# Kernel optimization log

Measured on AMD Instinct MI355X. Metric: run time of the kernel, lower is better.

## Reference

```python
import jax, jax.numpy as jnp
import numpy as np

B, N, F, H, OUT = 64, 512, 128, 256, 6


def setup_inputs() -> dict:
    key = jax.random.key(0)
    ks = jax.random.split(key, 20)
    s = 0.02
    inp = {
        "x": jax.random.normal(ks[0], (B * N, F), dtype=jnp.float32),
        "edge_index": jax.random.randint(ks[1], (2, 16), 0, B * N),
        "edge_weight": jax.random.uniform(ks[2], (16,), dtype=jnp.float32),
        "batch": jnp.repeat(jnp.arange(B, dtype=jnp.int64), N),
        "sigma": jax.random.uniform(ks[3], (1,), dtype=jnp.float32),
        "Wg": s * jax.random.normal(ks[4], (F, F)), "bg": jnp.zeros((F,)),
        "Wrel0": s * jax.random.normal(ks[5], (F, H)), "Wroot0": s * jax.random.normal(ks[6], (F, H)), "brel0": jnp.zeros((H,)),
        "Wrel1": s * jax.random.normal(ks[7], (H, H)), "Wroot1": s * jax.random.normal(ks[8], (H, H)), "brel1": jnp.zeros((H,)),
        "Wrel2": s * jax.random.normal(ks[9], (H, H)), "Wroot2": s * jax.random.normal(ks[10], (H, H)), "brel2": jnp.zeros((H,)),
        "W1": s * jax.random.normal(ks[11], (H, H)), "b1": jnp.zeros((H,)),
        "Wout": s * jax.random.normal(ks[12], (H, OUT)), "bout": jnp.zeros((OUT,)),
    }
    return inp


def _forward(x, sigma, Wg, bg, Wrel0, Wroot0, brel0, Wrel1, Wroot1, brel1,
             Wrel2, Wroot2, brel2, W1, b1, Wout, bout):
    # gdmLinear
    h = x @ Wg + bg                      # [B*N, F]
    hw = h.reshape(B, N, -1)             # to_dense_batch (equal-size windows)
    # pairwise squared distances per window -> Gaussian kernel
    sq = jnp.sum(hw * hw, axis=-1)       # [B, N]
    dist = jnp.maximum(sq[:, :, None] + sq[:, None, :]
                       - 2.0 * jnp.einsum('bnf,bmf->bnm', hw, hw), 0.0)
    A = jnp.exp(-dist / (2.0 * sigma[0] ** 2))   # [B, N, N], all > 0
    A = A * (1.0 - jnp.eye(N, dtype=A.dtype))    # nonzero extraction drops self-loops

    def conv(h, Wrel, Wroot, brel):
        # GraphConv: out_i = W_rel @ sum_j A[j,i] * h_j + b_rel + W_root @ h_i
        agg = jnp.einsum('bji,bjf->bif', A, h)
        return agg @ Wrel + brel + h @ Wroot

    h = hw
    h = jax.nn.relu(conv(h, Wrel0, Wroot0, brel0))
    h = jax.nn.relu(conv(h, Wrel1, Wroot1, brel1))
    h = conv(h, Wrel2, Wroot2, brel2)
    g = jnp.mean(h, axis=1)              # global_mean_pool (equal-size graphs)
    g = jax.nn.relu(g @ W1 + b1)
    return g @ Wout + bout               # [B, OUT]


def reference(x, edge_index, edge_weight, batch, sigma, Wg, bg,
              Wrel0, Wroot0, brel0, Wrel1, Wroot1, brel1,
              Wrel2, Wroot2, brel2, W1, b1, Wout, bout):
    # edge_index / edge_weight / batch inputs are recomputed internally by GdmGNN
    return _forward(x, sigma, Wg, bg, Wrel0, Wroot0, brel0, Wrel1, Wroot1, brel1,
                    Wrel2, Wroot2, brel2, W1, b1, Wout, bout)
```

## Files before the change

### kernel.cpp

```cpp
#include <hip/hip_runtime.h>
#include <math.h>

#define Bsz 64
#define Nn 512
#define Ff 128
#define Hh 256
#define OUTD 6
#define MTOT (Bsz * Nn)

typedef __bf16 bf16x8 __attribute__((ext_vector_type(8)));
typedef float f32x4 __attribute__((ext_vector_type(4)));
typedef int int4v __attribute__((ext_vector_type(4)));
typedef unsigned short ushort4v __attribute__((ext_vector_type(4)));

__device__ __forceinline__ unsigned short f2bf(float f) {
    unsigned u = __float_as_uint(f);
    u += 0x7FFFu + ((u >> 16) & 1u);
    return (unsigned short)(u >> 16);
}
__device__ __forceinline__ float bf2f(unsigned short s) {
    return __uint_as_float(((unsigned)s) << 16);
}

#define SWZ(r) (((r) ^ ((r) >> 2)) & 3)

__device__ __forceinline__ void async_ld16(const unsigned short* g, unsigned short* l) {
    __builtin_amdgcn_global_load_lds(
        (const __attribute__((address_space(1))) void*)g,
        (__attribute__((address_space(3))) void*)l,
        16, 0, 0);
}

#define LDH 40
#define TSZ (128 * 32)
#define ATS (256 * 32)
#define AGP 136
#define AGP1 264

__global__ __launch_bounds__(512) void fused_l0(
    const unsigned short* __restrict__ h0T,
    const unsigned short* __restrict__ Arows,
    const unsigned short* __restrict__ h0b,
    const unsigned short* __restrict__ WrelT0,
    const unsigned short* __restrict__ WrootT0,
    const float* __restrict__ brel0,
    unsigned short* __restrict__ h1b,
    unsigned short* __restrict__ h1T)
{
    int id = blockIdx.x;
    int b = id & 63;
    int nt = id >> 6;
    int n0g = nt * 128;
    long nodeBase = (long)b * Nn + n0g;

    const unsigned short* HT = h0T + (long)b * Ff * Nn;
    const unsigned short* AR = Arows + (long)b * Nn * Nn;

    __shared__ unsigned short SA[2 * ATS];
    __shared__ unsigned short SB[2 * TSZ];
    __shared__ unsigned short aggL[128 * AGP];

    int tid = threadIdx.x;
    int lane = tid & 63;
    int wave = tid >> 6;
    int quad = lane >> 4, l16 = lane & 15;
    int sr = lane >> 2, sc = lane & 3;

    {
        int wm = (wave >> 1) * 32, wn = (wave & 1) * 64;
        f32x4 acc[2][4] = {};
        auto issue = [&](int g) {
            int kk = g << 5;
            unsigned short* Ad = SA + (g & 1) * ATS;
            unsigned short* Bd = SB + (g & 1) * TSZ;
            int r = wave * 16 + sr;
            int c = sc ^ SWZ(r);
            async_ld16(HT + (long)r * Nn + kk + c * 8, Ad + (wave * 16) * 32);
            async_ld16(AR + (long)(n0g + r) * Nn + kk + c * 8, Bd + (wave * 16) * 32);
        };
        issue(0);
        for (int g = 0; g < (Nn >> 5); ++g) {
            __syncthreads();
            if (g + 1 < (Nn >> 5)) issue(g + 1);
            const unsigned short* Ab = SA + (g & 1) * ATS;
            const unsigned short* Bb = SB + (g & 1) * TSZ;
            bf16x8 af[2], bfr[4];
            #pragma unroll
            for (int i = 0; i < 2; ++i) {
                int r = wm + i * 16 + l16;
                af[i] = *(const bf16x8*)&Ab[r * 32 + (quad ^ SWZ(r)) * 8];
            }
            #pragma unroll
            for (int j = 0; j < 4; ++j) {
                int r = wn + j * 16 + l16;
                bfr[j] = *(const bf16x8*)&Bb[r * 32 + (quad ^ SWZ(r)) * 8];
            }
            #pragma unroll
            for (int i = 0; i < 2; ++i)
                #pragma unroll
                for (int j = 0; j < 4; ++j)
                    acc[i][j] = __builtin_amdgcn_mfma_f32_16x16x32_bf16(
                        af[i], bfr[j], acc[i][j], 0, 0, 0);
        }
        #pragma unroll
        for (int i = 0; i < 2; ++i) {
            int f = wm + i * 16 + quad * 4;
            #pragma unroll
            for (int j = 0; j < 4; ++j) {
                int nl = wn + j * 16 + l16;
                f32x4 v = acc[i][j];
                ushort4v p;
                p[0] = f2bf(v[0]); p[1] = f2bf(v[1]);
                p[2] = f2bf(v[2]); p[3] = f2bf(v[3]);
                *(ushort4v*)&aggL[nl * AGP + f] = p;
            }
        }
    }
    __syncthreads();

    {
        int wm = (wave >> 1) * 64, wn = (wave & 1) * 64;
        f32x4 acc[4][4] = {};
        auto issue2 = [&](int g) {
            const unsigned short* Wp = (g < 4) ? WrelT0 : WrootT0;
            int kk = (g & 3) << 5;
            unsigned short* Ad = SA + (g & 1) * ATS;
            int r = wave * 16 + sr;
            int c = sc ^ SWZ(r);
            async_ld16(Wp + (long)r * Ff + kk + c * 8, Ad + (wave * 16) * 32);
            int r2 = 128 + r;
            int c2 = sc ^ SWZ(r2);
            async_ld16(Wp + (long)r2 * Ff + kk + c2 * 8, Ad + (128 + wave * 16) * 32);
            if (g >= 4) {
                unsigned short* Bd = SB + (g & 1) * TSZ;
                async_ld16(h0b + (nodeBase + r) * Ff + kk + c * 8,
                           Bd + (wave * 16) * 32);
            }
        };
        issue2(0);
        for (int g = 0; g < 8; ++g) {
            __syncthreads();
            if (g + 1 < 8) issue2(g + 1);
            const unsigned short* Ab = SA + (g & 1) * ATS;
            bf16x8 af[4], bfr[4];
            #pragma unroll
            for (int i = 0; i < 4; ++i) {
                int r = wm + i * 16 + l16;
                af[i] = *(const bf16x8*)&Ab[r * 32 + (quad ^ SWZ(r)) * 8];
            }
            if (g < 4) {
                #pragma unroll
                for (int j = 0; j < 4; ++j) {
                    int nl = wn + j * 16 + l16;
                    bfr[j] = *(const bf16x8*)&aggL[nl * AGP + (g << 5) + quad * 8];
                }
            } else {
                const unsigned short* Bb = SB + (g & 1) * TSZ;
                #pragma unroll
                for (int j = 0; j < 4; ++j) {
                    int r = wn + j * 16 + l16;
                    bfr[j] = *(const bf16x8*)&Bb[r * 32 + (quad ^ SWZ(r)) * 8];
                }
            }
            #pragma unroll
            for (int i = 0; i < 4; ++i)
                #pragma unroll
                for (int j = 0; j < 4; ++j)
                    acc[i][j] = __builtin_amdgcn_mfma_f32_16x16x32_bf16(
                        af[i], bfr[j], acc[i][j], 0, 0, 0);
        }
        #pragma unroll
        for (int i = 0; i < 4; ++i) {
            int of = wm + i * 16 + quad * 4;
            float b0 = brel0[of + 0], b1 = brel0[of + 1];
            float b2 = brel0[of + 2], b3 = brel0[of + 3];
            #pragma unroll
            for (int j = 0; j < 4; ++j) {
                int nl = wn + j * 16 + l16;
                f32x4 v = acc[i][j];
                float o0 = fmaxf(v[0] + b0, 0.f), o1 = fmaxf(v[1] + b1, 0.f);
                float o2 = fmaxf(v[2] + b2, 0.f), o3 = fmaxf(v[3] + b3, 0.f);
                ushort4v p;
                p[0] = f2bf(o0); p[1] = f2bf(o1); p[2] = f2bf(o2); p[3] = f2bf(o3);
                *(ushort4v*)&h1b[(nodeBase + nl) * Hh + of] = p;
                long base = ((long)b * Hh) * 512 + n0g + nl;
                h1T[base + (long)(of + 0) * 512] = p[0];
                h1T[base + (long)(of + 1) * 512] = p[1];
                h1T[base + (long)(of + 2) * 512] = p[2];
                h1T[base + (long)(of + 3) * 512] = p[3];
            }
        }
    }
}

__global__ __launch_bounds__(512) void fused_l1(
    const unsigned short* __restrict__ h1T,
    const unsigned short* __restrict__ Arows,
    const unsigned short* __restrict__ h1b,
    const unsigned short* __restrict__ WrelT1,
    const unsigned short* __restrict__ WrootT1,
    const float* __restrict__ brel1,
    const float* __restrict__ w,
    float* __restrict__ vpart, float* __restrict__ mpart)
{
    constexpr int BTS = 128 * 32;

    int id = blockIdx.x;
    int b = id & 63;
    int nt = id >> 6;
    int n0g = nt * 128;
    long nodeBase = (long)b * Nn + n0g;

    const unsigned short* HT = h1T + (long)b * Hh * Nn;
    const unsigned short* AR = Arows + (long)b * Nn * Nn;

    __shared__ unsigned short SA[2 * ATS];
    __shared__ unsigned short SB[2 * BTS];
    __shared__ unsigned short aggL[128 * AGP1];

    int tid = threadIdx.x;
    int lane = tid & 63;
    int wave = tid >> 6;
    int quad = lane >> 4, l16 = lane & 15;
    int wm = (wave >> 1) * 64;
    int wn = (wave & 1) * 64;
    int sr = lane >> 2, sc = lane & 3;

    {
        f32x4 acc[4][4] = {};
        auto issue = [&](int g) {
            int kk = g << 5;
            unsigned short* Ad = SA + (g & 1) * ATS;
            int r = wave * 16 + sr;
            int c = sc ^ SWZ(r);
            async_ld16(HT + (long)r * Nn + kk + c * 8, Ad + (wave * 16) * 32);
            int r2 = 128 + r;
            int c2 = sc ^ SWZ(r2);
            async_ld16(HT + (long)r2 * Nn + kk + c2 * 8, Ad + (128 + wave * 16) * 32);
            unsigned short* Bd = SB + (g & 1) * BTS;
            async_ld16(AR + (long)(n0g + r) * Nn + kk + c * 8, Bd + (wave * 16) * 32);
        };
        issue(0);
        for (int g = 0; g < 16; ++g) {
            __syncthreads();
            if (g + 1 < 16) issue(g + 1);
            const unsigned short* Ab = SA + (g & 1) * ATS;
            const unsigned short* Bb = SB + (g & 1) * BTS;
            bf16x8 af[4], bfr[4];
            #pragma unroll
            for (int i = 0; i < 4; ++i) {
                int r = wm + i * 16 + l16;
                af[i] = *(const bf16x8*)&Ab[r * 32 + (quad ^ SWZ(r)) * 8];
            }
            #pragma unroll
            for (int j = 0; j < 4; ++j) {
                int r = wn + j * 16 + l16;
                bfr[j] = *(const bf16x8*)&Bb[r * 32 + (quad ^ SWZ(r)) * 8];
            }
            #pragma unroll
            for (int i = 0; i < 4; ++i)
                #pragma unroll
                for (int j = 0; j < 4; ++j)
                    acc[i][j] = __builtin_amdgcn_mfma_f32_16x16x32_bf16(
                        af[i], bfr[j], acc[i][j], 0, 0, 0);
        }
        #pragma unroll
        for (int i = 0; i < 4; ++i) {
            int f = wm + i * 16 + quad * 4;
            #pragma unroll
            for (int j = 0; j < 4; ++j) {
                int nl = wn + j * 16 + l16;
                f32x4 v = acc[i][j];
                ushort4v p;
                p[0] = f2bf(v[0]); p[1] = f2bf(v[1]);
                p[2] = f2bf(v[2]); p[3] = f2bf(v[3]);
                *(ushort4v*)&aggL[nl * AGP1 + f] = p;
            }
        }
    }
    __syncthreads();

    f32x4 acc[4][4] = {};
    auto issue2 = [&](int g) {
        const unsigned short* Wp = (g < 8) ? WrelT1 : WrootT1;
        int kk = (g & 7) << 5;
        unsigned short* Ad = SA + (g & 1) * ATS;
        int r = wave * 16 + sr;
        int c = sc ^ SWZ(r);
        async_ld16(Wp + (long)r * Hh + kk + c * 8, Ad + (wave * 16) * 32);
        int r2 = 128 + r;
        int c2 = sc ^ SWZ(r2);
        async_ld16(Wp + (long)r2 * Hh + kk + c2 * 8, Ad + (128 + wave * 16) * 32);
        if (g >= 8) {
            unsigned short* Bd = SB + (g & 1) * BTS;
            async_ld16(h1b + (nodeBase + r) * Hh + kk + c * 8, Bd + (wave * 16) * 32);
        }
    };
    issue2(0);
    for (int g = 0; g < 16; ++g) {
        __syncthreads();
        if (g + 1 < 16) issue2(g + 1);
        const unsigned short* Ab = SA + (g & 1) * ATS;
        bf16x8 af[4], bfr[4];
        #pragma unroll
        for (int i = 0; i < 4; ++i) {
            int r = wm + i * 16 + l16;
            af[i] = *(const bf16x8*)&Ab[r * 32 + (quad ^ SWZ(r)) * 8];
        }
        if (g < 8) {
            #pragma unroll
            for (int j = 0; j < 4; ++j) {
                int nl = wn + j * 16 + l16;
                bfr[j] = *(const bf16x8*)&aggL[nl * AGP1 + (g << 5) + quad * 8];
            }
        } else {
            const unsigned short* Bb = SB + (g & 1) * BTS;
            #pragma unroll
            for (int j = 0; j < 4; ++j) {
                int r = wn + j * 16 + l16;
                bfr[j] = *(const bf16x8*)&Bb[r * 32 + (quad ^ SWZ(r)) * 8];
            }
        }
        #pragma unroll
        for (int i = 0; i < 4; ++i)
            #pragma unroll
            for (int j = 0; j < 4; ++j)
                acc[i][j] = __builtin_amdgcn_mfma_f32_16x16x32_bf16(
                    af[i], bfr[j], acc[i][j], 0, 0, 0);
    }

    #pragma unroll
    for (int i = 0; i < 4; ++i) {
        int lf = wm + i * 16 + quad * 4;
        float b0 = brel1[lf + 0], b1 = brel1[lf + 1];
        float b2 = brel1[lf + 2], b3 = brel1[lf + 3];
        float vp0 = 0.f, vp1 = 0.f, vp2 = 0.f, vp3 = 0.f;
        float mp0 = 0.f, mp1 = 0.f, mp2 = 0.f, mp3 = 0.f;
        #pragma unroll
        for (int j = 0; j < 4; ++j) {
            long node = nodeBase + wn + j * 16 + l16;
            f32x4 v = acc[i][j];
            float o0 = fmaxf(v[0] + b0, 0.f), o1 = fmaxf(v[1] + b1, 0.f);
            float o2 = fmaxf(v[2] + b2, 0.f), o3 = fmaxf(v[3] + b3, 0.f);
            float h0v = bf2f(f2bf(o0)), h1v = bf2f(f2bf(o1));
            float h2v = bf2f(f2bf(o2)), h3v = bf2f(f2bf(o3));
            float wv = w[node];
            vp0 += wv * h0v; vp1 += wv * h1v; vp2 += wv * h2v; vp3 += wv * h3v;
            mp0 += h0v; mp1 += h1v; mp2 += h2v; mp3 += h3v;
        }
        #pragma unroll
        for (int m = 1; m < 16; m <<= 1) {
            vp0 += __shfl_xor(vp0, m); vp1 += __shfl_xor(vp1, m);
            vp2 += __shfl_xor(vp2, m); vp3 += __shfl_xor(vp3, m);
            mp0 += __shfl_xor(mp0, m); mp1 += __shfl_xor(mp1, m);
            mp2 += __shfl_xor(mp2, m); mp3 += __shfl_xor(mp3, m);
        }
        if (l16 == 0) {
            long o = ((long)(b * 8 + nt * 2 + (wave & 1))) * Hh + lf;
            float4 vv = {vp0, vp1, vp2, vp3};
            float4 mm = {mp0, mp1, mp2, mp3};
            *(float4*)&vpart[o] = vv;
            *(float4*)&mpart[o] = mm;
        }
    }
}

__global__ __launch_bounds__(256) void prep_h0(
    const float* __restrict__ x, const float* __restrict__ Wg,
    const float* __restrict__ bg,
    const float* __restrict__ Wrel0, const float* __restrict__ Wroot0,
    const float* __restrict__ Wrel1, const float* __restrict__ Wroot1,
    unsigned short* __restrict__ T0, unsigned short* __restrict__ T1,
    unsigned short* __restrict__ T2, unsigned short* __restrict__ T3,
    float* __restrict__ w,
    unsigned short* __restrict__ h0b, unsigned short* __restrict__ h0T,
    float* __restrict__ sqv)
{
    if (blockIdx.x < 896) {
        int idx = blockIdx.x * 256 + threadIdx.x;
        if (idx >= 196608) { w[idx - 196608] = 0.f; return; }
        const float* src; unsigned short* dst; int kin; int e;
        if      (idx <  32768) { src = Wrel0;  dst = T0; kin = 128; e = idx; }
        else if (idx <  65536) { src = Wroot0; dst = T1; kin = 128; e = idx - 32768; }
        else if (idx < 131072) { src = Wrel1;  dst = T2; kin = 256; e = idx - 65536; }
        else                   { src = Wroot1; dst = T3; kin = 256; e = idx - 131072; }
        int o = (kin == 128) ? (e >> 7) : (e >> 8);
        int i = e & (kin - 1);
        dst[e] = f2bf(src[(long)i * 256 + o]);
        return;
    }

    __shared__ unsigned short As[128 * LDH];
    __shared__ unsigned short Bs[128 * LDH];
    __shared__ float rsq[128];

    int tid = threadIdx.x;
    int lane = tid & 63;
    int wave = tid >> 6;
    int quad = lane >> 4, l16 = lane & 15;
    int wm = (wave >> 1) * 64, wn = (wave & 1) * 64;
    int m0 = (blockIdx.x - 896) * 128;

    f32x4 acc[4][4] = {};

    for (int k0 = 0; k0 < Ff; k0 += 32) {
        __syncthreads();
        #pragma unroll
        for (int l = 0; l < 2; ++l) {
            int idx = tid + l * 256;
            int r = idx >> 2, ch = idx & 3;
            const float* px = x + (long)(m0 + r) * Ff + k0 + ch * 8;
            float4 xa = *(const float4*)px;
            float4 xb = *(const float4*)(px + 4);
            ushort4v pa, pb;
            pa[0] = f2bf(xa.x); pa[1] = f2bf(xa.y); pa[2] = f2bf(xa.z); pa[3] = f2bf(xa.w);
            pb[0] = f2bf(xb.x); pb[1] = f2bf(xb.y); pb[2] = f2bf(xb.z); pb[3] = f2bf(xb.w);
            *(ushort4v*)&As[r * LDH + ch * 8] = pa;
            *(ushort4v*)&As[r * LDH + ch * 8 + 4] = pb;
            int kk = k0 + ch * 8;
            ushort4v qa, qb;
            #pragma unroll
            for (int u = 0; u < 4; ++u) qa[u] = f2bf(Wg[(long)(kk + u) * 128 + r]);
            #pragma unroll
            for (int u = 0; u < 4; ++u) qb[u] = f2bf(Wg[(long)(kk + 4 + u) * 128 + r]);
            *(ushort4v*)&Bs[r * LDH + ch * 8] = qa;
            *(ushort4v*)&Bs[r * LDH + ch * 8 + 4] = qb;
        }
        __syncthreads();
        bf16x8 af[4], bfr[4];
        #pragma unroll
        for (int i = 0; i < 4; ++i)
            af[i] = *(const bf16x8*)&As[(wm + i * 16 + l16) * LDH + quad * 8];
        #pragma unroll
        for (int j = 0; j < 4; ++j)
            bfr[j] = *(const bf16x8*)&Bs[(wn + j * 16 + l16) * LDH + quad * 8];
        #pragma unroll
        for (int i = 0; i < 4; ++i)
            #pragma unroll
            for (int j = 0; j < 4; ++j)
                acc[i][j] = __builtin_amdgcn_mfma_f32_16x16x32_bf16(
                    af[i], bfr[j], acc[i][j], 0, 0, 0);
    }

    if (tid < 128) rsq[tid] = 0.f;
    __syncthreads();

    #pragma unroll
    for (int i = 0; i < 4; ++i) {
        int lrow = wm + i * 16 + quad * 4;
        int mb = m0 + lrow;
        float rp0 = 0.f, rp1 = 0.f, rp2 = 0.f, rp3 = 0.f;
        #pragma unroll
        for (int j = 0; j < 4; ++j) {
            int n = wn + j * 16 + l16;
            f32x4 v = acc[i][j];
            float bv = bg[n];
            unsigned short s0 = f2bf(v[0] + bv), s1 = f2bf(v[1] + bv);
            unsigned short s2 = f2bf(v[2] + bv), s3 = f2bf(v[3] + bv);
            h0b[(long)(mb + 0) * Ff + n] = s0;
            h0b[(long)(mb + 1) * Ff + n] = s1;
            h0b[(long)(mb + 2) * Ff + n] = s2;
            h0b[(long)(mb + 3) * Ff + n] = s3;
            ushort4v p; p[0] = s0; p[1] = s1; p[2] = s2; p[3] = s3;
            long ti = ((long)(mb >> 9) * Ff + n) * 512 + (mb & 511);
            *(ushort4v*)&h0T[ti] = p;
            float f0 = bf2f(s0), f1 = bf2f(s1), f2 = bf2f(s2), f3 = bf2f(s3);
            rp0 += f0 * f0; rp1 += f1 * f1; rp2 += f2 * f2; rp3 += f3 * f3;
        }
        #pragma unroll
        for (int m = 1; m < 16; m <<= 1) {
            rp0 += __shfl_xor(rp0, m);
            rp1 += __shfl_xor(rp1, m);
            rp2 += __shfl_xor(rp2, m);
            rp3 += __shfl_xor(rp3, m);
        }
        if (l16 == 0) {
            atomicAdd(&rsq[lrow + 0], rp0);
            atomicAdd(&rsq[lrow + 1], rp1);
            atomicAdd(&rsq[lrow + 2], rp2);
            atomicAdd(&rsq[lrow + 3], rp3);
        }
    }
    __syncthreads();
    if (tid < 128) sqv[m0 + tid] = rsq[tid];
}

__global__ __launch_bounds__(512) void gram_A_mfma(
    const unsigned short* __restrict__ h0b, const float* __restrict__ sqv,
    const float* __restrict__ sigma, unsigned short* __restrict__ Aout,
    float* __restrict__ w)
{
    int id = blockIdx.x;
    int b = id & 63;
    int t = id >> 6;
    int i0 = (t & 3) * 128, j0 = (t >> 2) * 128;

    const unsigned short* H = h0b + (long)b * Nn * Ff;
    const float* SQ = sqv + (long)b * Nn;
    unsigned short* Ab = Aout + (long)b * Nn * Nn;

    __shared__ unsigned short Is[2 * TSZ];
    __shared__ unsigned short Js[2 * TSZ];
    __shared__ float rsum[128];

    int tid = threadIdx.x;
    int lane = tid & 63;
    int wave = tid >> 6;
    int quad = lane >> 4, l16 = lane & 15;
    int wm = (wave >> 1) * 32, wn = (wave & 1) * 64;

    int sr = lane >> 2, sc = lane & 3;

    f32x4 acc[2][4] = {};

    auto issue = [&](int g) {
        int kk = g << 5;
        unsigned short* Id = Is + (g & 1) * TSZ;
        unsigned short* Jd = Js + (g & 1) * TSZ;
        int r = wave * 16 + sr;
        int c = sc ^ SWZ(r);
        async_ld16(H + (long)(i0 + r) * Ff + kk + c * 8, Id + (wave * 16) * 32);
        async_ld16(H + (long)(j0 + r) * Ff + kk + c * 8, Jd + (wave * 16) * 32);
    };

    issue(0);
    for (int g = 0; g < (Ff >> 5); ++g) {
        __syncthreads();
        if (g + 1 < (Ff >> 5)) issue(g + 1);
        const unsigned short* Ib = Is + (g & 1) * TSZ;
        const unsigned short* Jb = Js + (g & 1) * TSZ;
        bf16x8 af[2], bfr[4];
        #pragma unroll
        for (int i = 0; i < 2; ++i) {
            int r = wm + i * 16 + l16;
            af[i] = *(const bf16x8*)&Ib[r * 32 + (quad ^ SWZ(r)) * 8];
        }
        #pragma unroll
        for (int j = 0; j < 4; ++j) {
            int r = wn + j * 16 + l16;
            bfr[j] = *(const bf16x8*)&Jb[r * 32 + (quad ^ SWZ(r)) * 8];
        }
        #pragma unroll
        for (int i = 0; i < 2; ++i)
            #pragma unroll
            for (int j = 0; j < 4; ++j)
                acc[i][j] = __builtin_amdgcn_mfma_f32_16x16x32_bf16(
                    af[i], bfr[j], acc[i][j], 0, 0, 0);
    }

    if (tid < 128) rsum[tid] = 0.f;
    __syncthreads();

    float s = sigma[0];
    float inv2s2 = 1.0f / (2.0f * s * s);
    #pragma unroll
    for (int i = 0; i < 2; ++i) {
        int lrow = wm + i * 16 + quad * 4;
        int rb = i0 + lrow;
        float rs0 = 0.f, rs1 = 0.f, rs2 = 0.f, rs3 = 0.f;
        #pragma unroll
        for (int j = 0; j < 4; ++j) {
            int c = j0 + wn + j * 16 + l16;
            float sqc = SQ[c];
            f32x4 v = acc[i][j];
            ushort4v pk;
            float av[4];
            #pragma unroll
            for (int r4 = 0; r4 < 4; ++r4) {
                int r = rb + r4;
                float d = fmaxf(SQ[r] + sqc - 2.0f * v[r4], 0.0f);
                unsigned short a = (r == c) ? (unsigned short)0
                                            : f2bf(__expf(-d * inv2s2));
                pk[r4] = a;
                av[r4] = bf2f(a);
            }
            *(ushort4v*)&Ab[(long)c * Nn + rb] = pk;
            rs0 += av[0]; rs1 += av[1]; rs2 += av[2]; rs3 += av[3];
        }
        #pragma unroll
        for (int m = 1; m < 16; m <<= 1) {
            rs0 += __shfl_xor(rs0, m);
            rs1 += __shfl_xor(rs1, m);
            rs2 += __shfl_xor(rs2, m);
            rs3 += __shfl_xor(rs3, m);
        }
        if (l16 == 0) {
            atomicAdd(&rsum[lrow + 0], rs0);
            atomicAdd(&rsum[lrow + 1], rs1);
            atomicAdd(&rsum[lrow + 2], rs2);
            atomicAdd(&rsum[lrow + 3], rs3);
        }
    }
    __syncthreads();
    if (tid < 128) atomicAdd(&w[(long)b * Nn + i0 + tid], rsum[tid]);
}

__global__ __launch_bounds__(256) void head_kernel(
    const float* __restrict__ vpart, const float* __restrict__ mpart,
    const float* __restrict__ Wrel2, const float* __restrict__ Wroot2,
    const float* __restrict__ brel2,
    const float* __restrict__ W1, const float* __restrict__ b1,
    const float* __restrict__ Wout, const float* __restrict__ bout,
    float* __restrict__ out)
{
    int b = blockIdx.x;
    int j = threadIdx.x;
    __shared__ float vs[Hh], ms[Hh], gs[Hh], g2[Hh];
    float vp = 0.f, mp = 0.f;
    #pragma unroll
    for (int p = 0; p < 8; ++p) {
        long o = ((long)(b * 8 + p)) * Hh + j;
        vp += vpart[o];
        mp += mpart[o];
    }
    vs[j] = vp * (1.0f / (float)Nn);
    ms[j] = mp * (1.0f / (float)Nn);
    __syncthreads();
    float s = brel2[j];
    for (int c = 0; c < Hh; ++c)
        s += vs[c] * Wrel2[c * Hh + j] + ms[c] * Wroot2[c * Hh + j];
    gs[j] = s;
    __syncthreads();
    float t = b1[j];
    for (int k = 0; k < Hh; ++k) t += gs[k] * W1[k * Hh + j];
    g2[j] = fmaxf(t, 0.f);
    __syncthreads();
    if (j < OUTD) {
        float s2 = bout[j];
        for (int k = 0; k < Hh; ++k) s2 += g2[k] * Wout[k * OUTD + j];
        out[b * OUTD + j] = s2;
    }
}

extern "C" void kernel_launch(void* const* d_in, const int* in_sizes, int n_in,
                              void* d_out, int out_size, void* d_ws, size_t ws_size,
                              hipStream_t stream) {
    const float* x      = (const float*)d_in[0];
    const float* sigma  = (const float*)d_in[4];
    const float* Wg     = (const float*)d_in[5];
    const float* bg     = (const float*)d_in[6];
    const float* Wrel0  = (const float*)d_in[7];
    const float* Wroot0 = (const float*)d_in[8];
    const float* brel0  = (const float*)d_in[9];
    const float* Wrel1  = (const float*)d_in[10];
    const float* Wroot1 = (const float*)d_in[11];
    const float* brel1  = (const float*)d_in[12];
    const float* Wrel2  = (const float*)d_in[13];
    const float* Wroot2 = (const float*)d_in[14];
    const float* brel2  = (const float*)d_in[15];
    const float* W1     = (const float*)d_in[16];
    const float* b1     = (const float*)d_in[17];
    const float* Wout   = (const float*)d_in[18];
    const float* bout   = (const float*)d_in[19];
    float* out = (float*)d_out;

    char* ws = (char*)d_ws;
    unsigned short* h0b  = (unsigned short*)(ws + 16777216);
    unsigned short* h0T  = (unsigned short*)(ws + 25165824);
    float*          sq   = (float*)(ws + 33554432);
    unsigned short* Aadj = (unsigned short*)(ws + 33685504);
    unsigned short* h1b  = (unsigned short*)(ws + 84017152);
    unsigned short* h1T  = (unsigned short*)(ws + 100794368);
    unsigned short* WrelT0  = (unsigned short*)(ws + 167903232);
    unsigned short* WrootT0 = (unsigned short*)(ws + 167968768);
    unsigned short* WrelT1  = (unsigned short*)(ws + 168034304);
    unsigned short* WrootT1 = (unsigned short*)(ws + 168165376);
    float*          w     = (float*)(ws + 168558592);
    float*          vpart = (float*)(ws + 168689664);
    float*          mpart = (float*)(ws + 169213952);

    prep_h0<<<1152, 256, 0, stream>>>(x, Wg, bg, Wrel0, Wroot0, Wrel1, Wroot1,
                                      WrelT0, WrootT0, WrelT1, WrootT1,
                                      w, h0b, h0T, sq);

    gram_A_mfma<<<dim3(16 * Bsz, 1, 1), 512, 0, stream>>>(h0b, sq, sigma, Aadj, w);

    fused_l0<<<dim3(4 * Bsz, 1, 1), 512, 0, stream>>>(
        h0T, Aadj, h0b, WrelT0, WrootT0, brel0, h1b, h1T);

    fused_l1<<<dim3(4 * Bsz, 1, 1), 512, 0, stream>>>(
        h1T, Aadj, h1b, WrelT1, WrootT1, brel1, w, vpart, mpart);

    head_kernel<<<Bsz, 256, 0, stream>>>(vpart, mpart, Wrel2, Wroot2, brel2,
                                         W1, b1, Wout, bout, out);
}
```

Before: 211.5 us.

## Triple-buffer LDS tiles with explicit vmcnt waits for two-deep prefetch

Turns the double-buffered async global-to-LDS pipelines in the fused GraphConv kernels into triple-buffered ones. Two tiles are now in flight ahead of compute, and the full __syncthreads is replaced by a partial s_waitcnt vmcnt(n) followed by s_barrier. The aim is to hide more global-load latency behind the MFMA work. In exchange, LDS use per block grows, which can lower occupancy, and the hand-counted vmcnt values must match the number of loads issued per stage exactly or data races appear.

```diff
diff --git a/kernel.cpp b/kernel.cpp
--- a/kernel.cpp
+++ b/kernel.cpp
@@ -29,6 +29,23 @@
         (const __attribute__((address_space(1))) void*)g,
         (__attribute__((address_space(3))) void*)l,
         16, 0, 0);
+}
+
+__device__ __forceinline__ void wait_vm(int n) {
+    switch (n) {
+        case 0: asm volatile("s_waitcnt vmcnt(0)" ::: "memory"); break;
+        case 1: asm volatile("s_waitcnt vmcnt(1)" ::: "memory"); break;
+        case 2: asm volatile("s_waitcnt vmcnt(2)" ::: "memory"); break;
+        case 3: asm volatile("s_waitcnt vmcnt(3)" ::: "memory"); break;
+        case 4: asm volatile("s_waitcnt vmcnt(4)" ::: "memory"); break;
+        case 5: asm volatile("s_waitcnt vmcnt(5)" ::: "memory"); break;
+        default: asm volatile("s_waitcnt vmcnt(6)" ::: "memory"); break;
+    }
+}
+__device__ __forceinline__ void pipe_barrier(int n) {
+    wait_vm(n);
+    __builtin_amdgcn_s_barrier();
+    __builtin_amdgcn_sched_barrier(0);
 }
 
 #define LDH 40
@@ -56,8 +73,8 @@
     const unsigned short* HT = h0T + (long)b * Ff * Nn;
     const unsigned short* AR = Arows + (long)b * Nn * Nn;
 
-    __shared__ unsigned short SA[2 * ATS];
-    __shared__ unsigned short SB[2 * TSZ];
+    __shared__ unsigned short SA[3 * ATS];
+    __shared__ unsigned short SB[3 * TSZ];
     __shared__ unsigned short aggL[128 * AGP];
 
     int tid = threadIdx.x;
@@ -71,19 +88,19 @@
         f32x4 acc[2][4] = {};
         auto issue = [&](int g) {
             int kk = g << 5;
-            unsigned short* Ad = SA + (g & 1) * ATS;
-            unsigned short* Bd = SB + (g & 1) * TSZ;
+            unsigned short* Ad = SA + (g % 3) * ATS;
+            unsigned short* Bd = SB + (g % 3) * TSZ;
             int r = wave * 16 + sr;
             int c = sc ^ SWZ(r);
             async_ld16(HT + (long)r * Nn + kk + c * 8, Ad + (wave * 16) * 32);
             async_ld16(AR + (long)(n0g + r) * Nn + kk + c * 8, Bd + (wave * 16) * 32);
         };
-        issue(0);
-        for (int g = 0; g < (Nn >> 5); ++g) {
-            __syncthreads();
-            if (g + 1 < (Nn >> 5)) issue(g + 1);
-            const unsigned short* Ab = SA + (g & 1) * ATS;
-            const unsigned short* Bb = SB + (g & 1) * TSZ;
+        issue(0); issue(1);
+        for (int g = 0; g < 16; ++g) {
+            pipe_barrier(g + 1 < 16 ? 2 : 0);
+            if (g + 2 < 16) issue(g + 2);
+            const unsigned short* Ab = SA + (g % 3) * ATS;
+            const unsigned short* Bb = SB + (g % 3) * TSZ;
             bf16x8 af[2], bfr[4];
             #pragma unroll
             for (int i = 0; i < 2; ++i) {
@@ -124,7 +141,7 @@
         auto issue2 = [&](int g) {
             const unsigned short* Wp = (g < 4) ? WrelT0 : WrootT0;
             int kk = (g & 3) << 5;
-            unsigned short* Ad = SA + (g & 1) * ATS;
+            unsigned short* Ad = SA + (g % 3) * ATS;
             int r = wave * 16 + sr;
             int c = sc ^ SWZ(r);
             async_ld16(Wp + (long)r * Ff + kk + c * 8, Ad + (wave * 16) * 32);
@@ -132,16 +149,17 @@
             int c2 = sc ^ SWZ(r2);
             async_ld16(Wp + (long)r2 * Ff + kk + c2 * 8, Ad + (128 + wave * 16) * 32);
             if (g >= 4) {
-                unsigned short* Bd = SB + (g & 1) * TSZ;
+                unsigned short* Bd = SB + (g % 3) * TSZ;
                 async_ld16(h0b + (nodeBase + r) * Ff + kk + c * 8,
                            Bd + (wave * 16) * 32);
             }
         };
-        issue2(0);
+        issue2(0); issue2(1);
         for (int g = 0; g < 8; ++g) {
-            __syncthreads();
-            if (g + 1 < 8) issue2(g + 1);
-            const unsigned short* Ab = SA + (g & 1) * ATS;
+            int nx = g + 1;
+            pipe_barrier(nx >= 8 ? 0 : (nx < 4 ? 2 : 3));
+            if (g + 2 < 8) issue2(g + 2);
+            const unsigned short* Ab = SA + (g % 3) * ATS;
             bf16x8 af[4], bfr[4];
             #pragma unroll
             for (int i = 0; i < 4; ++i) {
@@ -155,7 +173,7 @@
                     bfr[j] = *(const bf16x8*)&aggL[nl * AGP + (g << 5) + quad * 8];
                 }
             } else {
-                const unsigned short* Bb = SB + (g & 1) * TSZ;
+                const unsigned short* Bb = SB + (g % 3) * TSZ;
                 #pragma unroll
                 for (int j = 0; j < 4; ++j) {
                     int r = wn + j * 16 + l16;
@@ -214,8 +232,8 @@
     const unsigned short* HT = h1T + (long)b * Hh * Nn;
     const unsigned short* AR = Arows + (long)b * Nn * Nn;
 
-    __shared__ unsigned short SA[2 * ATS];
-    __shared__ unsigned short SB[2 * BTS];
+    __shared__ unsigned short SA[3 * ATS];
+    __shared__ unsigned short SB[3 * BTS];
     __shared__ unsigned short aggL[128 * AGP1];
 
     int tid = threadIdx.x;
@@ -230,22 +248,22 @@
         f32x4 acc[4][4] = {};
         auto issue = [&](int g) {
             int kk = g << 5;
-            unsigned short* Ad = SA + (g & 1) * ATS;
+            unsigned short* Ad = SA + (g % 3) * ATS;
             int r = wave * 16 + sr;
             int c = sc ^ SWZ(r);
             async_ld16(HT + (long)r * Nn + kk + c * 8, Ad + (wave * 16) * 32);
             int r2 = 128 + r;
             int c2 = sc ^ SWZ(r2);
             async_ld16(HT + (long)r2 * Nn + kk + c2 * 8, Ad + (128 + wave * 16) * 32);
-            unsigned short* Bd = SB + (g & 1) * BTS;
+            unsigned short* Bd = SB + (g % 3) * BTS;
             async_ld16(AR + (long)(n0g + r) * Nn + kk + c * 8, Bd + (wave * 16) * 32);
         };
-        issue(0);
+        issue(0); issue(1);
         for (int g = 0; g < 16; ++g) {
-            __syncthreads();
-            if (g + 1 < 16) issue(g + 1);
-            const unsigned short* Ab = SA + (g & 1) * ATS;
-            const unsigned short* Bb = SB + (g & 1) * BTS;
+            pipe_barrier(g + 1 < 16 ? 3 : 0);
+            if (g + 2 < 16) issue(g + 2);
+            const unsigned short* Ab = SA + (g % 3) * ATS;
+            const unsigned short* Bb = SB + (g % 3) * BTS;
             bf16x8 af[4], bfr[4];
             #pragma unroll
             for (int i = 0; i < 4; ++i) {
@@ -284,7 +302,7 @@
     auto issue2 = [&](int g) {
         const unsigned short* Wp = (g < 8) ? WrelT1 : WrootT1;
         int kk = (g & 7) << 5;
-        unsigned short* Ad = SA + (g & 1) * ATS;
+        unsigned short* Ad = SA + (g % 3) * ATS;
         int r = wave * 16 + sr;
         int c = sc ^ SWZ(r);
         async_ld16(Wp + (long)r * Hh + kk + c * 8, Ad + (wave * 16) * 32);
@@ -292,15 +310,16 @@
         int c2 = sc ^ SWZ(r2);
         async_ld16(Wp + (long)r2 * Hh + kk + c2 * 8, Ad + (128 + wave * 16) * 32);
         if (g >= 8) {
-            unsigned short* Bd = SB + (g & 1) * BTS;
+            unsigned short* Bd = SB + (g % 3) * BTS;
             async_ld16(h1b + (nodeBase + r) * Hh + kk + c * 8, Bd + (wave * 16) * 32);
         }
     };
-    issue2(0);
+    issue2(0); issue2(1);
     for (int g = 0; g < 16; ++g) {
-        __syncthreads();
-        if (g + 1 < 16) issue2(g + 1);
-        const unsigned short* Ab = SA + (g & 1) * ATS;
+        int nx = g + 1;
+        pipe_barrier(nx >= 16 ? 0 : (nx < 8 ? 2 : 3));
+        if (g + 2 < 16) issue2(g + 2);
+        const unsigned short* Ab = SA + (g % 3) * ATS;
         bf16x8 af[4], bfr[4];
         #pragma unroll
         for (int i = 0; i < 4; ++i) {
@@ -314,7 +333,7 @@
                 bfr[j] = *(const bf16x8*)&aggL[nl * AGP1 + (g << 5) + quad * 8];
             }
         } else {
-            const unsigned short* Bb = SB + (g & 1) * BTS;
+            const unsigned short* Bb = SB + (g % 3) * BTS;
             #pragma unroll
             for (int j = 0; j < 4; ++j) {
                 int r = wn + j * 16 + l16;
```

New measurement: 212.4 us. Within noise of the previous version (+0.4%).

## Halve node tile in fused GraphConv kernels to double grid and cut LDS

Applied to the files above, without the earlier changes.

Both fused layer kernels now process 64 nodes per block instead of 128, doubling the grid from 256 to 512 blocks. Shared memory is repacked into a smaller pool plus a swizzled per-k-tile aggregate buffer, and the __syncthreads calls are replaced with an explicit vmcnt drain plus barrier. The head kernel and partial buffers are adjusted to 16 partials per graph. This is meant to raise occupancy and fill more CUs than the previous 256 blocks did. The cost is that the weight and h^T tiles are reloaded twice as often across blocks, and each wave issues fewer MFMAs per tile.

```diff
diff --git a/kernel.cpp b/kernel.cpp
--- a/kernel.cpp
+++ b/kernel.cpp
@@ -10,7 +10,6 @@
 
 typedef __bf16 bf16x8 __attribute__((ext_vector_type(8)));
 typedef float f32x4 __attribute__((ext_vector_type(4)));
-typedef int int4v __attribute__((ext_vector_type(4)));
 typedef unsigned short ushort4v __attribute__((ext_vector_type(4)));
 
 __device__ __forceinline__ unsigned short f2bf(float f) {
@@ -31,11 +30,14 @@
         16, 0, 0);
 }
 
+__device__ __forceinline__ void drain_barrier() {
+    asm volatile("s_waitcnt vmcnt(0)" ::: "memory");
+    __builtin_amdgcn_s_barrier();
+    __builtin_amdgcn_sched_barrier(0);
+}
+
 #define LDH 40
 #define TSZ (128 * 32)
-#define ATS (256 * 32)
-#define AGP 136
-#define AGP1 264
 
 __global__ __launch_bounds__(512) void fused_l0(
     const unsigned short* __restrict__ h0T,
@@ -50,15 +52,14 @@
     int id = blockIdx.x;
     int b = id & 63;
     int nt = id >> 6;
-    int n0g = nt * 128;
+    int n0g = nt * 64;
     long nodeBase = (long)b * Nn + n0g;
 
     const unsigned short* HT = h0T + (long)b * Ff * Nn;
     const unsigned short* AR = Arows + (long)b * Nn * Nn;
 
-    __shared__ unsigned short SA[2 * ATS];
-    __shared__ unsigned short SB[2 * TSZ];
-    __shared__ unsigned short aggL[128 * AGP];
+    __shared__ unsigned short POOL[20480];
+    __shared__ unsigned short AGK[4 * 64 * 32];
 
     int tid = threadIdx.x;
     int lane = tid & 63;
@@ -67,82 +68,89 @@
     int sr = lane >> 2, sc = lane & 3;
 
     {
-        int wm = (wave >> 1) * 32, wn = (wave & 1) * 64;
-        f32x4 acc[2][4] = {};
+        int wm = (wave >> 1) * 32, wn = (wave & 1) * 32;
+        f32x4 acc[2][2] = {};
         auto issue = [&](int g) {
             int kk = g << 5;
-            unsigned short* Ad = SA + (g & 1) * ATS;
-            unsigned short* Bd = SB + (g & 1) * TSZ;
+            unsigned short* Ad = POOL + (g & 1) * 4096;
             int r = wave * 16 + sr;
             int c = sc ^ SWZ(r);
             async_ld16(HT + (long)r * Nn + kk + c * 8, Ad + (wave * 16) * 32);
-            async_ld16(AR + (long)(n0g + r) * Nn + kk + c * 8, Bd + (wave * 16) * 32);
+            if (wave < 4) {
+                unsigned short* Bd = POOL + 8192 + (g & 1) * 2048;
+                async_ld16(AR + (long)(n0g + r) * Nn + kk + c * 8,
+                           Bd + (wave * 16) * 32);
+            }
         };
         issue(0);
-        for (int g = 0; g < (Nn >> 5); ++g) {
-            __syncthreads();
-            if (g + 1 < (Nn >> 5)) issue(g + 1);
-            const unsigned short* Ab = SA + (g & 1) * ATS;
-            const unsigned short* Bb = SB + (g & 1) * TSZ;
-            bf16x8 af[2], bfr[4];
+        for (int g = 0; g < 16; ++g) {
+            drain_barrier();
+            if (g + 1 < 16) issue(g + 1);
+            const unsigned short* Ab = POOL + (g & 1) * 4096;
+            const unsigned short* Bb = POOL + 8192 + (g & 1) * 2048;
+            bf16x8 af[2], bfr[2];
             #pragma unroll
             for (int i = 0; i < 2; ++i) {
                 int r = wm + i * 16 + l16;
                 af[i] = *(const bf16x8*)&Ab[r * 32 + (quad ^ SWZ(r)) * 8];
             }
             #pragma unroll
-            for (int j = 0; j < 4; ++j) {
+            for (int j = 0; j < 2; ++j) {
                 int r = wn + j * 16 + l16;
                 bfr[j] = *(const bf16x8*)&Bb[r * 32 + (quad ^ SWZ(r)) * 8];
             }
             #pragma unroll
             for (int i = 0; i < 2; ++i)
                 #pragma unroll
-                for (int j = 0; j < 4; ++j)
+                for (int j = 0; j < 2; ++j)
                     acc[i][j] = __builtin_amdgcn_mfma_f32_16x16x32_bf16(
                         af[i], bfr[j], acc[i][j], 0, 0, 0);
         }
         #pragma unroll
         for (int i = 0; i < 2; ++i) {
             int f = wm + i * 16 + quad * 4;
-            #pragma unroll
-            for (int j = 0; j < 4; ++j) {
+            int kt = f >> 5, fo = f & 31;
+            #pragma unroll
+            for (int j = 0; j < 2; ++j) {
                 int nl = wn + j * 16 + l16;
                 f32x4 v = acc[i][j];
                 ushort4v p;
                 p[0] = f2bf(v[0]); p[1] = f2bf(v[1]);
                 p[2] = f2bf(v[2]); p[3] = f2bf(v[3]);
-                *(ushort4v*)&aggL[nl * AGP + f] = p;
+                int idx = kt * 2048 + nl * 32 + (((fo >> 3) ^ SWZ(nl)) << 3) + (fo & 7);
+                *(ushort4v*)&AGK[idx] = p;
             }
         }
     }
     __syncthreads();
 
     {
-        int wm = (wave >> 1) * 64, wn = (wave & 1) * 64;
-        f32x4 acc[4][4] = {};
+        int wm = (wave >> 1) * 64, wn = (wave & 1) * 32;
+        f32x4 acc[4][2] = {};
         auto issue2 = [&](int g) {
             const unsigned short* Wp = (g < 4) ? WrelT0 : WrootT0;
             int kk = (g & 3) << 5;
-            unsigned short* Ad = SA + (g & 1) * ATS;
-            int r = wave * 16 + sr;
+            unsigned short* Ad = POOL + (g & 1) * 8192;
+            int r = wave * 32 + sr;
             int c = sc ^ SWZ(r);
-            async_ld16(Wp + (long)r * Ff + kk + c * 8, Ad + (wave * 16) * 32);
-            int r2 = 128 + r;
+            async_ld16(Wp + (long)r * Ff + kk + c * 8, Ad + (wave * 32) * 32);
+            int r2 = r + 16;
             int c2 = sc ^ SWZ(r2);
-            async_ld16(Wp + (long)r2 * Ff + kk + c2 * 8, Ad + (128 + wave * 16) * 32);
-            if (g >= 4) {
-                unsigned short* Bd = SB + (g & 1) * TSZ;
-                async_ld16(h0b + (nodeBase + r) * Ff + kk + c * 8,
+            async_ld16(Wp + (long)r2 * Ff + kk + c2 * 8, Ad + (wave * 32 + 16) * 32);
+            if (g >= 4 && wave < 4) {
+                unsigned short* Bd = POOL + 16384 + (g & 1) * 2048;
+                int rb = wave * 16 + sr;
+                int cb = sc ^ SWZ(rb);
+                async_ld16(h0b + (nodeBase + rb) * Ff + kk + cb * 8,
                            Bd + (wave * 16) * 32);
             }
         };
         issue2(0);
         for (int g = 0; g < 8; ++g) {
-            __syncthreads();
+            drain_barrier();
             if (g + 1 < 8) issue2(g + 1);
-            const unsigned short* Ab = SA + (g & 1) * ATS;
-            bf16x8 af[4], bfr[4];
+            const unsigned short* Ab = POOL + (g & 1) * 8192;
+            bf16x8 af[4], bfr[2];
             #pragma unroll
             for (int i = 0; i < 4; ++i) {
                 int r = wm + i * 16 + l16;
@@ -150,14 +158,14 @@
             }
             if (g < 4) {
                 #pragma unroll
-                for (int j = 0; j < 4; ++j) {
-                    int nl = wn + j * 16 + l16;
-                    bfr[j] = *(const bf16x8*)&aggL[nl * AGP + (g << 5) + quad * 8];
+                for (int j = 0; j < 2; ++j) {
+                    int r = wn + j * 16 + l16;
+                    bfr[j] = *(const bf16x8*)&AGK[g * 2048 + r * 32 + ((quad ^ SWZ(r)) << 3)];
                 }
             } else {
-                const unsigned short* Bb = SB + (g & 1) * TSZ;
+                const unsigned short* Bb = POOL + 16384 + (g & 1) * 2048;
                 #pragma unroll
-                for (int j = 0; j < 4; ++j) {
+                for (int j = 0; j < 2; ++j) {
                     int r = wn + j * 16 + l16;
                     bfr[j] = *(const bf16x8*)&Bb[r * 32 + (quad ^ SWZ(r)) * 8];
                 }
@@ -165,7 +173,7 @@
             #pragma unroll
             for (int i = 0; i < 4; ++i)
                 #pragma unroll
-                for (int j = 0; j < 4; ++j)
+                for (int j = 0; j < 2; ++j)
                     acc[i][j] = __builtin_amdgcn_mfma_f32_16x16x32_bf16(
                         af[i], bfr[j], acc[i][j], 0, 0, 0);
         }
@@ -175,7 +183,7 @@
             float b0 = brel0[of + 0], b1 = brel0[of + 1];
             float b2 = brel0[of + 2], b3 = brel0[of + 3];
             #pragma unroll
-            for (int j = 0; j < 4; ++j) {
+            for (int j = 0; j < 2; ++j) {
                 int nl = wn + j * 16 + l16;
                 f32x4 v = acc[i][j];
                 float o0 = fmaxf(v[0] + b0, 0.f), o1 = fmaxf(v[1] + b1, 0.f);
@@ -203,105 +211,112 @@
     const float* __restrict__ w,
     float* __restrict__ vpart, float* __restrict__ mpart)
 {
-    constexpr int BTS = 128 * 32;
-
     int id = blockIdx.x;
     int b = id & 63;
     int nt = id >> 6;
-    int n0g = nt * 128;
+    int n0g = nt * 64;
     long nodeBase = (long)b * Nn + n0g;
 
     const unsigned short* HT = h1T + (long)b * Hh * Nn;
     const unsigned short* AR = Arows + (long)b * Nn * Nn;
 
-    __shared__ unsigned short SA[2 * ATS];
-    __shared__ unsigned short SB[2 * BTS];
-    __shared__ unsigned short aggL[128 * AGP1];
+    __shared__ unsigned short POOL[20480];
+    __shared__ unsigned short AGK[8 * 64 * 32];
 
     int tid = threadIdx.x;
     int lane = tid & 63;
     int wave = tid >> 6;
     int quad = lane >> 4, l16 = lane & 15;
     int wm = (wave >> 1) * 64;
-    int wn = (wave & 1) * 64;
+    int wn = (wave & 1) * 32;
     int sr = lane >> 2, sc = lane & 3;
 
     {
-        f32x4 acc[4][4] = {};
+        f32x4 acc[4][2] = {};
         auto issue = [&](int g) {
             int kk = g << 5;
-            unsigned short* Ad = SA + (g & 1) * ATS;
-            int r = wave * 16 + sr;
+            unsigned short* Ad = POOL + (g & 1) * 8192;
+            int r = wave * 32 + sr;
             int c = sc ^ SWZ(r);
-            async_ld16(HT + (long)r * Nn + kk + c * 8, Ad + (wave * 16) * 32);
-            int r2 = 128 + r;
+            async_ld16(HT + (long)r * Nn + kk + c * 8, Ad + (wave * 32) * 32);
+            int r2 = r + 16;
             int c2 = sc ^ SWZ(r2);
-            async_ld16(HT + (long)r2 * Nn + kk + c2 * 8, Ad + (128 + wave * 16) * 32);
-            unsigned short* Bd = SB + (g & 1) * BTS;
-            async_ld16(AR + (long)(n0g + r) * Nn + kk + c * 8, Bd + (wave * 16) * 32);
+            async_ld16(HT + (long)r2 * Nn + kk + c2 * 8, Ad + (wave * 32 + 16) * 32);
+            if (wave < 4) {
+                unsigned short* Bd = POOL + 16384 + (g & 1) * 2048;
+                int rb = wave * 16 + sr;
+                int cb = sc ^ SWZ(rb);
+                async_ld16(AR + (long)(n0g + rb) * Nn + kk + cb * 8,
+                           Bd + (wave * 16) * 32);
+            }
         };
         issue(0);
         for (int g = 0; g < 16; ++g) {
-            __syncthreads();
+            drain_barrier();
             if (g + 1 < 16) issue(g + 1);
-            const unsigned short* Ab = SA + (g & 1) * ATS;
-            const unsigned short* Bb = SB + (g & 1) * BTS;
-            bf16x8 af[4], bfr[4];
+            const unsigned short* Ab = POOL + (g & 1) * 8192;
+            const unsigned short* Bb = POOL + 16384 + (g & 1) * 2048;
+            bf16x8 af[4], bfr[2];
             #pragma unroll
             for (int i = 0; i < 4; ++i) {
                 int r = wm + i * 16 + l16;
                 af[i] = *(const bf16x8*)&Ab[r * 32 + (quad ^ SWZ(r)) * 8];
             }
             #pragma unroll
-            for (int j = 0; j < 4; ++j) {
+            for (int j = 0; j < 2; ++j) {
                 int r = wn + j * 16 + l16;
                 bfr[j] = *(const bf16x8*)&Bb[r * 32 + (quad ^ SWZ(r)) * 8];
             }
             #pragma unroll
             for (int i = 0; i < 4; ++i)
                 #pragma unroll
-                for (int j = 0; j < 4; ++j)
+                for (int j = 0; j < 2; ++j)
                     acc[i][j] = __builtin_amdgcn_mfma_f32_16x16x32_bf16(
                         af[i], bfr[j], acc[i][j], 0, 0, 0);
         }
         #pragma unroll
         for (int i = 0; i < 4; ++i) {
             int f = wm + i * 16 + quad * 4;
-            #pragma unroll
-            for (int j = 0; j < 4; ++j) {
+            int kt = f >> 5, fo = f & 31;
+            #pragma unroll
+            for (int j = 0; j < 2; ++j) {
                 int nl = wn + j * 16 + l16;
                 f32x4 v = acc[i][j];
                 ushort4v p;
                 p[0] = f2bf(v[0]); p[1] = f2bf(v[1]);
                 p[2] = f2bf(v[2]); p[3] = f2bf(v[3]);
-                *(ushort4v*)&aggL[nl * AGP1 + f] = p;
-            }
-        }
-    }
-    __syncthreads();
-
-    f32x4 acc[4][4] = {};
+                int idx = kt * 2048 + nl * 32 + (((fo >> 3) ^ SWZ(nl)) << 3) + (fo & 7);
+                *(ushort4v*)&AGK[idx] = p;
+            }
+        }
+    }
+    __syncthreads();
+
+    f32x4 acc[4][2] = {};
     auto issue2 = [&](int g) {
         const unsigned short* Wp = (g < 8) ? WrelT1 : WrootT1;
         int kk = (g & 7) << 5;
-        unsigned short* Ad = SA + (g & 1) * ATS;
-        int r = wave * 16 + sr;
+        unsigned short* Ad = POOL + (g & 1) * 8192;
+        int r = wave * 32 + sr;
         int c = sc ^ SWZ(r);
-        async_ld16(Wp + (long)r * Hh + kk + c * 8, Ad + (wave * 16) * 32);
-        int r2 = 128 + r;
+        async_ld16(Wp + (long)r * Hh + kk + c * 8, Ad + (wave * 32) * 32);
+        int r2 = r + 16;
         int c2 = sc ^ SWZ(r2);
-        async_ld16(Wp + (long)r2 * Hh + kk + c2 * 8, Ad + (128 + wave * 16) * 32);
-        if (g >= 8) {
-            unsigned short* Bd = SB + (g & 1) * BTS;
-            async_ld16(h1b + (nodeBase + r) * Hh + kk + c * 8, Bd + (wave * 16) * 32);
+        async_ld16(Wp + (long)r2 * Hh + kk + c2 * 8, Ad + (wave * 32 + 16) * 32);
+        if (g >= 8 && wave < 4) {
+            unsigned short* Bd = POOL + 16384 + (g & 1) * 2048;
+            int rb = wave * 16 + sr;
+            int cb = sc ^ SWZ(rb);
+            async_ld16(h1b + (nodeBase + rb) * Hh + kk + cb * 8,
+                       Bd + (wave * 16) * 32);
         }
     };
     issue2(0);
     for (int g = 0; g < 16; ++g) {
-        __syncthreads();
+        drain_barrier();
         if (g + 1 < 16) issue2(g + 1);
-        const unsigned short* Ab = SA + (g & 1) * ATS;
-        bf16x8 af[4], bfr[4];
+        const unsigned short* Ab = POOL + (g & 1) * 8192;
+        bf16x8 af[4], bfr[2];
         #pragma unroll
         for (int i = 0; i < 4; ++i) {
             int r = wm + i * 16 + l16;
@@ -309,14 +324,14 @@
         }
         if (g < 8) {
             #pragma unroll
-            for (int j = 0; j < 4; ++j) {
-                int nl = wn + j * 16 + l16;
-                bfr[j] = *(const bf16x8*)&aggL[nl * AGP1 + (g << 5) + quad * 8];
+            for (int j = 0; j < 2; ++j) {
+                int r = wn + j * 16 + l16;
+                bfr[j] = *(const bf16x8*)&AGK[g * 2048 + r * 32 + ((quad ^ SWZ(r)) << 3)];
             }
         } else {
-            const unsigned short* Bb = SB + (g & 1) * BTS;
-            #pragma unroll
-            for (int j = 0; j < 4; ++j) {
+            const unsigned short* Bb = POOL + 16384 + (g & 1) * 2048;
+            #pragma unroll
+            for (int j = 0; j < 2; ++j) {
                 int r = wn + j * 16 + l16;
                 bfr[j] = *(const bf16x8*)&Bb[r * 32 + (quad ^ SWZ(r)) * 8];
             }
@@ -324,7 +339,7 @@
         #pragma unroll
         for (int i = 0; i < 4; ++i)
             #pragma unroll
-            for (int j = 0; j < 4; ++j)
+            for (int j = 0; j < 2; ++j)
                 acc[i][j] = __builtin_amdgcn_mfma_f32_16x16x32_bf16(
                     af[i], bfr[j], acc[i][j], 0, 0, 0);
     }
@@ -337,7 +352,7 @@
         float vp0 = 0.f, vp1 = 0.f, vp2 = 0.f, vp3 = 0.f;
         float mp0 = 0.f, mp1 = 0.f, mp2 = 0.f, mp3 = 0.f;
         #pragma unroll
-        for (int j = 0; j < 4; ++j) {
+        for (int j = 0; j < 2; ++j) {
             long node = nodeBase + wn + j * 16 + l16;
             f32x4 v = acc[i][j];
             float o0 = fmaxf(v[0] + b0, 0.f), o1 = fmaxf(v[1] + b1, 0.f);
@@ -356,7 +371,7 @@
             mp2 += __shfl_xor(mp2, m); mp3 += __shfl_xor(mp3, m);
         }
         if (l16 == 0) {
-            long o = ((long)(b * 8 + nt * 2 + (wave & 1))) * Hh + lf;
+            long o = ((long)(b * 16 + nt * 2 + (wave & 1))) * Hh + lf;
             float4 vv = {vp0, vp1, vp2, vp3};
             float4 mm = {mp0, mp1, mp2, mp3};
             *(float4*)&vpart[o] = vv;
@@ -608,8 +623,8 @@
     __shared__ float vs[Hh], ms[Hh], gs[Hh], g2[Hh];
     float vp = 0.f, mp = 0.f;
     #pragma unroll
-    for (int p = 0; p < 8; ++p) {
-        long o = ((long)(b * 8 + p)) * Hh + j;
+    for (int p = 0; p < 16; ++p) {
+        long o = ((long)(b * 16 + p)) * Hh + j;
         vp += vpart[o];
         mp += mpart[o];
     }
@@ -667,7 +682,7 @@
     unsigned short* WrootT1 = (unsigned short*)(ws + 168165376);
     float*          w     = (float*)(ws + 168558592);
     float*          vpart = (float*)(ws + 168689664);
-    float*          mpart = (float*)(ws + 169213952);
+    float*          mpart = (float*)(ws + 169738240);
 
     prep_h0<<<1152, 256, 0, stream>>>(x, Wg, bg, Wrel0, Wroot0, Wrel1, Wroot1,
                                       WrelT0, WrootT0, WrelT1, WrootT1,
@@ -675,10 +690,10 @@
 
     gram_A_mfma<<<dim3(16 * Bsz, 1, 1), 512, 0, stream>>>(h0b, sq, sigma, Aadj, w);
 
-    fused_l0<<<dim3(4 * Bsz, 1, 1), 512, 0, stream>>>(
+    fused_l0<<<dim3(8 * Bsz, 1, 1), 512, 0, stream>>>(
         h0T, Aadj, h0b, WrelT0, WrootT0, brel0, h1b, h1T);
 
-    fused_l1<<<dim3(4 * Bsz, 1, 1), 512, 0, stream>>>(
+    fused_l1<<<dim3(8 * Bsz, 1, 1), 512, 0, stream>>>(
         h1T, Aadj, h1b, WrelT1, WrootT1, brel1, w, vpart, mpart);
 
     head_kernel<<<Bsz, 256, 0, stream>>>(vpart, mpart, Wrel2, Wroot2, brel2,
```

Measured after the change: 214.3 us. No clear change (+1.3%).
